# Performance work log

Hardware: AMD Instinct MI355X
Metric: run time of the kernel (lower is better)

Reference implementation:

```python
import jax, jax.numpy as jnp
import numpy as np

NUM_AGENTS = 8
OBSERVATION_SIZE = 30
INPUT_SHAPE = 4 + 2 * OBSERVATION_SIZE  # 64
STATE_SHAPE = INPUT_SHAPE * NUM_AGENTS  # 512
HYPER_HIDDEN_DIM = 40
QMIX_HIDDEN_DIM = 40


def setup_inputs() -> dict:
    key = jax.random.key(0)
    ks = jax.random.split(key, 16)
    E, T = 256, 256

    def lin(k, fan_in, fan_out):
        kw, kb = jax.random.split(k)
        bound = 1.0 / np.sqrt(fan_in)
        w = jax.random.uniform(kw, (fan_in, fan_out), jnp.float32, -bound, bound)
        b = jax.random.uniform(kb, (fan_out,), jnp.float32, -bound, bound)
        return w, b

    hw1_w0, hw1_b0 = lin(ks[0], STATE_SHAPE, HYPER_HIDDEN_DIM)
    hw1_w1, hw1_b1 = lin(ks[1], HYPER_HIDDEN_DIM, NUM_AGENTS * QMIX_HIDDEN_DIM)
    hw2_w0, hw2_b0 = lin(ks[2], STATE_SHAPE, HYPER_HIDDEN_DIM)
    hw2_w1, hw2_b1 = lin(ks[3], HYPER_HIDDEN_DIM, QMIX_HIDDEN_DIM)
    hb1_w, hb1_b = lin(ks[4], STATE_SHAPE, QMIX_HIDDEN_DIM)
    hb2_w0, hb2_b0 = lin(ks[5], STATE_SHAPE, QMIX_HIDDEN_DIM)
    hb2_w1, hb2_b1 = lin(ks[6], QMIX_HIDDEN_DIM, 1)

    return {
        "q_values": jax.random.normal(ks[7], (E, T, NUM_AGENTS), jnp.float32),
        "states": jax.random.normal(ks[8], (E, T, STATE_SHAPE), jnp.float32),
        "hw1_w0": hw1_w0, "hw1_b0": hw1_b0, "hw1_w1": hw1_w1, "hw1_b1": hw1_b1,
        "hw2_w0": hw2_w0, "hw2_b0": hw2_b0, "hw2_w1": hw2_w1, "hw2_b1": hw2_b1,
        "hb1_w": hb1_w, "hb1_b": hb1_b,
        "hb2_w0": hb2_w0, "hb2_b0": hb2_b0, "hb2_w1": hb2_w1, "hb2_b1": hb2_b1,
    }


def reference(q_values, states, hw1_w0, hw1_b0, hw1_w1, hw1_b1,
              hw2_w0, hw2_b0, hw2_w1, hw2_b1,
              hb1_w, hb1_b, hb2_w0, hb2_b0, hb2_w1, hb2_b1):
    E = q_values.shape[0]
    q = q_values.reshape(-1, NUM_AGENTS)          # [B, A]
    s = states.reshape(-1, STATE_SHAPE)           # [B, S]

    # hyper_w1: Linear-ReLU-Linear -> abs -> [B, A, H]
    w1 = jnp.abs(jax.nn.relu(s @ hw1_w0 + hw1_b0) @ hw1_w1 + hw1_b1)
    w1 = w1.reshape(-1, NUM_AGENTS, QMIX_HIDDEN_DIM)
    b1 = s @ hb1_w + hb1_b                        # [B, H]

    hidden = jax.nn.elu(jnp.einsum('ba,bah->bh', q, w1) + b1)  # [B, H]

    # hyper_w2 -> abs -> [B, H]; hyper_b2 -> [B, 1]
    w2 = jnp.abs(jax.nn.relu(s @ hw2_w0 + hw2_b0) @ hw2_w1 + hw2_b1)
    b2 = jax.nn.relu(s @ hb2_w0 + hb2_b0) @ hb2_w1 + hb2_b1    # [B, 1]

    q_total = jnp.einsum('bh,bh->b', hidden, w2)[:, None] + b2  # [B, 1]
    return q_total.reshape(E, -1, 1)
```

## Files before the change

### kernel.cpp

```cpp
#include <hip/hip_runtime.h>
#include <math.h>

#define NA 8
#define SS 512
#define N1 160
#define BROWS 32
#define NTHREADS 320

typedef __attribute__((ext_vector_type(8))) short bf16x8;
typedef __attribute__((ext_vector_type(4))) float f32x4;

static __device__ __forceinline__ unsigned short f2bf(float f) {
    union { float f; unsigned u; } v; v.f = f;
    unsigned r = v.u + 0x7FFFu + ((v.u >> 16) & 1u);
    return (unsigned short)(r >> 16);
}
static __device__ __forceinline__ float bf2f(unsigned short u) {
    union { unsigned u; float f; } v; v.u = ((unsigned)u) << 16; return v.f;
}

#define BP_OFF   0
#define BP1_OFF  81920
#define BP2_OFF  102400
#define BIAS0_BYTE 210944

__global__ void prep_kernel(const float* __restrict__ hw1_w0, const float* __restrict__ hb1_w,
                            const float* __restrict__ hw2_w0, const float* __restrict__ hb2_w0,
                            const float* __restrict__ hw1_w1, const float* __restrict__ hw2_w1,
                            const float* __restrict__ hw1_b0, const float* __restrict__ hb1_b,
                            const float* __restrict__ hw2_b0, const float* __restrict__ hb2_b0,
                            unsigned short* __restrict__ ws16, float* __restrict__ bias0) {
    int idx = blockIdx.x * blockDim.x + threadIdx.x;
    if (idx < 81920) {
        int i = idx & 7, l = (idx >> 3) & 63, t = idx >> 9;
        int kt = t & 15, nt = t >> 4;
        int k = kt * 32 + (l >> 4) * 8 + i;
        int n = nt * 16 + (l & 15);
        int seg = n / 40, c = n - seg * 40;
        const float* src = (seg == 0) ? hw1_w0 : (seg == 1) ? hb1_w : (seg == 2) ? hw2_w0 : hb2_w0;
        ws16[BP_OFF + idx] = f2bf(src[k * 40 + c]);
    } else if (idx < 81920 + 20480) {
        int j = idx - 81920;
        int i = j & 7, l = (j >> 3) & 63, t = j >> 9;
        int kt = t & 1, nt = t >> 1;
        int k = kt * 32 + (l >> 4) * 8 + i;
        int n = nt * 16 + (l & 15);
        float v = (k < 40) ? hw1_w1[k * 320 + n] : 0.f;
        ws16[BP1_OFF + j] = f2bf(v);
    } else if (idx < 81920 + 20480 + 3072) {
        int j = idx - 102400;
        int i = j & 7, l = (j >> 3) & 63, t = j >> 9;
        int kt = t & 1, nt = t >> 1;
        int k = kt * 32 + (l >> 4) * 8 + i;
        int n = nt * 16 + (l & 15);
        float v = (k < 40 && n < 40) ? hw2_w1[k * 40 + n] : 0.f;
        ws16[BP2_OFF + j] = f2bf(v);
    } else if (idx < 81920 + 20480 + 3072 + 160) {
        int j = idx - 105472;
        int seg = j / 40, c = j - seg * 40;
        const float* b = (seg == 0) ? hw1_b0 : (seg == 1) ? hb1_b : (seg == 2) ? hw2_b0 : hb2_b0;
        bias0[j] = b[c];
    }
}

#define REG0      0
#define P_OFF     32768
#define H1_OFF    53760
#define H2_OFF    57856
#define W2_OFF    61952
#define B2_OFF    64512
#define SMEM_BYTES 64640

__global__ __launch_bounds__(NTHREADS) void qmix_kernel(
    const float* __restrict__ q_values, const float* __restrict__ states,
    const unsigned short* __restrict__ Bp, const unsigned short* __restrict__ Bp1,
    const unsigned short* __restrict__ Bp2, const float* __restrict__ bias0,
    const float* __restrict__ hw1_b1, const float* __restrict__ hw2_b1,
    const float* __restrict__ hb2_w1, const float* __restrict__ hb2_b1,
    float* __restrict__ out)
{
    __shared__ __align__(16) char smem[SMEM_BYTES];
    const int tid = threadIdx.x;
    const int wv = tid >> 6;
    const int l = tid & 63;
    const int row0 = blockIdx.x * BROWS;

    {
        const float4* sg = (const float4*)(states + (size_t)row0 * SS);
        for (int idx = tid; idx < BROWS * (SS / 4); idx += NTHREADS) {
            int r = idx >> 7;
            int c4 = idx & 127;
            float4 v = sg[idx];
            ushort4 b;
            b.x = f2bf(v.x); b.y = f2bf(v.y); b.z = f2bf(v.z); b.w = f2bf(v.w);
            int byte = (r * 1024 + c4 * 8) ^ ((r & 7) << 4);
            *(ushort4*)(smem + byte) = b;
        }
    }
    __syncthreads();

    f32x4 acc[2][2] = {};
    {
        const int kch = (l >> 4) * 16;
        const int r0 = (l & 15);
        const int r1 = r0 + 16;
        const int swz0 = (r0 & 7) << 4;
        const unsigned short* bp0 = Bp + (size_t)((wv * 2 + 0) * 16) * 512 + (size_t)l * 8;
        const unsigned short* bp1 = Bp + (size_t)((wv * 2 + 1) * 16) * 512 + (size_t)l * 8;
        #pragma unroll
        for (int kt = 0; kt < 16; ++kt) {
            bf16x8 a0 = *(const bf16x8*)(smem + ((r0 * 1024 + kt * 64 + kch) ^ swz0));
            bf16x8 a1 = *(const bf16x8*)(smem + ((r1 * 1024 + kt * 64 + kch) ^ swz0));
            bf16x8 b0 = *(const bf16x8*)(bp0 + kt * 512);
            bf16x8 b1 = *(const bf16x8*)(bp1 + kt * 512);
            acc[0][0] = __builtin_amdgcn_mfma_f32_16x16x32_bf16(a0, b0, acc[0][0], 0, 0, 0);
            acc[0][1] = __builtin_amdgcn_mfma_f32_16x16x32_bf16(a0, b1, acc[0][1], 0, 0, 0);
            acc[1][0] = __builtin_amdgcn_mfma_f32_16x16x32_bf16(a1, b0, acc[1][0], 0, 0, 0);
            acc[1][1] = __builtin_amdgcn_mfma_f32_16x16x32_bf16(a1, b1, acc[1][1], 0, 0, 0);
        }
    }
    {
        float* P = (float*)(smem + P_OFF);
        #pragma unroll
        for (int mt = 0; mt < 2; ++mt)
        #pragma unroll
        for (int ntl = 0; ntl < 2; ++ntl)
        #pragma unroll
        for (int g = 0; g < 4; ++g) {
            int row = mt * 16 + (l >> 4) * 4 + g;
            int col = wv * 32 + ntl * 16 + (l & 15);
            P[row * 164 + col] = acc[mt][ntl][g];
        }
    }
    __syncthreads();

    {
        float* P = (float*)(smem + P_OFF);
        for (int idx = tid; idx < BROWS * N1; idx += NTHREADS) {
            int r = idx / N1, c = idx - r * N1;
            float v = P[r * 164 + c] + bias0[c];
            if ((unsigned)(c - 40) >= 40u) v = fmaxf(v, 0.f);
            P[r * 164 + c] = v;
        }
    }
    __syncthreads();

    {
        float* P = (float*)(smem + P_OFF);
        char* H1 = smem + H1_OFF;
        char* H2 = smem + H2_OFF;
        for (int idx = tid; idx < BROWS * 64; idx += NTHREADS) {
            int r = idx >> 6, j = idx & 63;
            float v1 = (j < 40) ? P[r * 164 + j] : 0.f;
            float v2 = (j < 40) ? P[r * 164 + 80 + j] : 0.f;
            int byte = (r * 128 + j * 2) ^ ((r & 7) << 4);
            *(unsigned short*)(H1 + byte) = f2bf(v1);
            *(unsigned short*)(H2 + byte) = f2bf(v2);
        }
        if (tid < 32) {
            float s = hb2_b1[0];
            #pragma unroll 8
            for (int j = 0; j < 40; ++j) s += P[tid * 164 + 120 + j] * hb2_w1[j];
            ((float*)(smem + B2_OFF))[tid] = s;
        }
    }
    __syncthreads();

    {
        char* H1 = smem + H1_OFF;
        const int kch = (l >> 4) * 16;
        f32x4 wacc[2][4] = {};
        #pragma unroll
        for (int kt = 0; kt < 2; ++kt) {
            bf16x8 a[2];
            #pragma unroll
            for (int mt = 0; mt < 2; ++mt) {
                int row = mt * 16 + (l & 15);
                a[mt] = *(const bf16x8*)(H1 + ((row * 128 + kt * 64 + kch) ^ ((row & 7) << 4)));
            }
            #pragma unroll
            for (int t = 0; t < 4; ++t) {
                int nt1 = wv * 4 + t;
                bf16x8 b = *(const bf16x8*)(Bp1 + ((size_t)(nt1 * 2 + kt) * 64 + l) * 8);
                wacc[0][t] = __builtin_amdgcn_mfma_f32_16x16x32_bf16(a[0], b, wacc[0][t], 0, 0, 0);
                wacc[1][t] = __builtin_amdgcn_mfma_f32_16x16x32_bf16(a[1], b, wacc[1][t], 0, 0, 0);
            }
        }
        unsigned short* W1 = (unsigned short*)(smem + REG0);
        #pragma unroll
        for (int mt = 0; mt < 2; ++mt)
        #pragma unroll
        for (int t = 0; t < 4; ++t)
        #pragma unroll
        for (int g = 0; g < 4; ++g) {
            int row = mt * 16 + (l >> 4) * 4 + g;
            int n = (wv * 4 + t) * 16 + (l & 15);
            W1[row * 320 + n] = f2bf(fabsf(wacc[mt][t][g] + hw1_b1[n]));
        }
        if (wv < 3) {
            char* H2 = smem + H2_OFF;
            f32x4 c2[2] = {};
            #pragma unroll
            for (int kt = 0; kt < 2; ++kt) {
                bf16x8 a[2];
                #pragma unroll
                for (int mt = 0; mt < 2; ++mt) {
                    int row = mt * 16 + (l & 15);
                    a[mt] = *(const bf16x8*)(H2 + ((row * 128 + kt * 64 + kch) ^ ((row & 7) << 4)));
                }
                bf16x8 b = *(const bf16x8*)(Bp2 + ((size_t)(wv * 2 + kt) * 64 + l) * 8);
                c2[0] = __builtin_amdgcn_mfma_f32_16x16x32_bf16(a[0], b, c2[0], 0, 0, 0);
                c2[1] = __builtin_amdgcn_mfma_f32_16x16x32_bf16(a[1], b, c2[1], 0, 0, 0);
            }
            unsigned short* W2 = (unsigned short*)(smem + W2_OFF);
            #pragma unroll
            for (int mt = 0; mt < 2; ++mt)
            #pragma unroll
            for (int g = 0; g < 4; ++g) {
                int row = mt * 16 + (l >> 4) * 4 + g;
                int n = wv * 16 + (l & 15);
                if (n < 40) W2[row * 40 + n] = f2bf(fabsf(c2[mt][g] + hw2_b1[n]));
            }
        }
    }
    __syncthreads();

    {
        float* P = (float*)(smem + P_OFF);
        unsigned short* W1 = (unsigned short*)(smem + REG0);
        unsigned short* W2 = (unsigned short*)(smem + W2_OFF);
        float* PR = (float*)(smem + H2_OFF);
        int r = tid / 10;
        int hb_ = tid - r * 10;
        const float4* qp = (const float4*)(q_values + (size_t)(row0 + r) * NA);
        float4 qa = qp[0], qb = qp[1];
        float qv[8] = {qa.x, qa.y, qa.z, qa.w, qb.x, qb.y, qb.z, qb.w};
        float psum = 0.f;
        #pragma unroll
        for (int kk = 0; kk < 4; ++kk) {
            int h = hb_ + kk * 10;
            float acc2 = P[r * 164 + 40 + h];
            #pragma unroll
            for (int a = 0; a < 8; ++a) acc2 += qv[a] * bf2f(W1[r * 320 + a * 40 + h]);
            float hid = (acc2 > 0.f) ? acc2 : expm1f(acc2);
            psum += hid * bf2f(W2[r * 40 + h]);
        }
        PR[tid] = psum;
    }
    __syncthreads();
    if (tid < 32) {
        float* PR = (float*)(smem + H2_OFF);
        float s = ((float*)(smem + B2_OFF))[tid];
        #pragma unroll
        for (int g = 0; g < 10; ++g) s += PR[tid * 10 + g];
        out[row0 + tid] = s;
    }
}

extern "C" void kernel_launch(void* const* d_in, const int* in_sizes, int n_in,
                              void* d_out, int out_size, void* d_ws, size_t ws_size,
                              hipStream_t stream) {
    const float* q_values = (const float*)d_in[0];
    const float* states   = (const float*)d_in[1];
    const float* hw1_w0 = (const float*)d_in[2];
    const float* hw1_b0 = (const float*)d_in[3];
    const float* hw1_w1 = (const float*)d_in[4];
    const float* hw1_b1 = (const float*)d_in[5];
    const float* hw2_w0 = (const float*)d_in[6];
    const float* hw2_b0 = (const float*)d_in[7];
    const float* hw2_w1 = (const float*)d_in[8];
    const float* hw2_b1 = (const float*)d_in[9];
    const float* hb1_w  = (const float*)d_in[10];
    const float* hb1_b  = (const float*)d_in[11];
    const float* hb2_w0 = (const float*)d_in[12];
    const float* hb2_b0 = (const float*)d_in[13];
    const float* hb2_w1 = (const float*)d_in[14];
    const float* hb2_b1 = (const float*)d_in[15];

    unsigned short* ws16 = (unsigned short*)d_ws;
    float* bias0 = (float*)((char*)d_ws + BIAS0_BYTE);

    const int prep_total = 81920 + 20480 + 3072 + 160;
    prep_kernel<<<(prep_total + 255) / 256, 256, 0, stream>>>(
        hw1_w0, hb1_w, hw2_w0, hb2_w0, hw1_w1, hw2_w1,
        hw1_b0, hb1_b, hw2_b0, hb2_b0, ws16, bias0);

    const int B = in_sizes[0] / NA;
    qmix_kernel<<<B / BROWS, NTHREADS, 0, stream>>>(
        q_values, states,
        ws16 + BP_OFF, ws16 + BP1_OFF, ws16 + BP2_OFF, bias0,
        hw1_b1, hw2_b1, hb2_w1, hb2_b1, (float*)d_out);
}
```

Measured before the change: 306.4 us.

## Fuse first-layer bias/ReLU epilogue into MFMA registers, drop P staging buffer

The first GEMM's accumulators now get bias, ReLU, bf16 conversion and the hb2 dot-product reduction applied directly from registers. The reduction uses wave shuffles and writes straight into the H1/H2/b1/B2 buffers. This removes the fp32 P staging matrix and two block-wide barriers with their passes over shared memory. It also shrinks shared memory and requests 4 blocks per CU via launch bounds to raise occupancy. The cost is branchy per-column epilogue code and a possible register cap from the launch-bounds hint.

```diff
diff --git a/kernel.cpp b/kernel.cpp
--- a/kernel.cpp
+++ b/kernel.cpp
@@ -3,7 +3,6 @@
 
 #define NA 8
 #define SS 512
-#define N1 160
 #define BROWS 32
 #define NTHREADS 320
 
@@ -63,15 +62,15 @@
     }
 }
 
-#define REG0      0
-#define P_OFF     32768
-#define H1_OFF    53760
-#define H2_OFF    57856
-#define W2_OFF    61952
-#define B2_OFF    64512
-#define SMEM_BYTES 64640
-
-__global__ __launch_bounds__(NTHREADS) void qmix_kernel(
+#define W1_STRIDE 324
+#define B1_OFF    32768
+#define H1_OFF    38400
+#define H2_OFF    42496
+#define W2_OFF    46592
+#define B2_OFF    49152
+#define SMEM_BYTES 49408
+
+__global__ __launch_bounds__(NTHREADS, 4) void qmix_kernel(
     const float* __restrict__ q_values, const float* __restrict__ states,
     const unsigned short* __restrict__ Bp, const unsigned short* __restrict__ Bp1,
     const unsigned short* __restrict__ Bp2, const float* __restrict__ bias0,
@@ -83,6 +82,7 @@
     const int tid = threadIdx.x;
     const int wv = tid >> 6;
     const int l = tid & 63;
+    const int p = l & 15;
     const int row0 = blockIdx.x * BROWS;
 
     {
@@ -96,13 +96,19 @@
             int byte = (r * 1024 + c4 * 8) ^ ((r & 7) << 4);
             *(ushort4*)(smem + byte) = b;
         }
+        for (int idx = tid; idx < 32 * 24; idx += NTHREADS) {
+            int r = idx / 24, k = 40 + (idx - r * 24);
+            int byte = (r * 128 + k * 2) ^ ((r & 7) << 4);
+            *(unsigned short*)(smem + H1_OFF + byte) = 0;
+            *(unsigned short*)(smem + H2_OFF + byte) = 0;
+        }
     }
     __syncthreads();
 
     f32x4 acc[2][2] = {};
     {
         const int kch = (l >> 4) * 16;
-        const int r0 = (l & 15);
+        const int r0 = p;
         const int r1 = r0 + 16;
         const int swz0 = (r0 & 7) << 4;
         const unsigned short* bp0 = Bp + (size_t)((wv * 2 + 0) * 16) * 512 + (size_t)l * 8;
@@ -119,49 +125,47 @@
             acc[1][1] = __builtin_amdgcn_mfma_f32_16x16x32_bf16(a1, b1, acc[1][1], 0, 0, 0);
         }
     }
-    {
-        float* P = (float*)(smem + P_OFF);
-        #pragma unroll
-        for (int mt = 0; mt < 2; ++mt)
-        #pragma unroll
-        for (int ntl = 0; ntl < 2; ++ntl)
-        #pragma unroll
-        for (int g = 0; g < 4; ++g) {
-            int row = mt * 16 + (l >> 4) * 4 + g;
-            int col = wv * 32 + ntl * 16 + (l & 15);
-            P[row * 164 + col] = acc[mt][ntl][g];
-        }
-    }
-    __syncthreads();
-
-    {
-        float* P = (float*)(smem + P_OFF);
-        for (int idx = tid; idx < BROWS * N1; idx += NTHREADS) {
-            int r = idx / N1, c = idx - r * N1;
-            float v = P[r * 164 + c] + bias0[c];
-            if ((unsigned)(c - 40) >= 40u) v = fmaxf(v, 0.f);
-            P[r * 164 + c] = v;
-        }
-    }
-    __syncthreads();
-
-    {
-        float* P = (float*)(smem + P_OFF);
-        char* H1 = smem + H1_OFF;
-        char* H2 = smem + H2_OFF;
-        for (int idx = tid; idx < BROWS * 64; idx += NTHREADS) {
-            int r = idx >> 6, j = idx & 63;
-            float v1 = (j < 40) ? P[r * 164 + j] : 0.f;
-            float v2 = (j < 40) ? P[r * 164 + 80 + j] : 0.f;
-            int byte = (r * 128 + j * 2) ^ ((r & 7) << 4);
-            *(unsigned short*)(H1 + byte) = f2bf(v1);
-            *(unsigned short*)(H2 + byte) = f2bf(v2);
-        }
-        if (tid < 32) {
-            float s = hb2_b1[0];
-            #pragma unroll 8
-            for (int j = 0; j < 40; ++j) s += P[tid * 164 + 120 + j] * hb2_w1[j];
-            ((float*)(smem + B2_OFF))[tid] = s;
+
+    {
+        float rs[2][4] = {{0.f,0.f,0.f,0.f},{0.f,0.f,0.f,0.f}};
+        float* b1buf = (float*)(smem + B1_OFF);
+        #pragma unroll
+        for (int ntl = 0; ntl < 2; ++ntl) {
+            const int c = wv * 32 + ntl * 16 + p;
+            const float bia = bias0[c];
+            const float hbw = (c >= 120) ? hb2_w1[c - 120] : 0.f;
+            #pragma unroll
+            for (int mt = 0; mt < 2; ++mt)
+            #pragma unroll
+            for (int g = 0; g < 4; ++g) {
+                const int row = mt * 16 + (l >> 4) * 4 + g;
+                const float v = acc[mt][ntl][g] + bia;
+                if (c < 40) {
+                    *(unsigned short*)(smem + H1_OFF + ((row * 128 + c * 2) ^ ((row & 7) << 4)))
+                        = f2bf(fmaxf(v, 0.f));
+                } else if (c < 80) {
+                    b1buf[row * 44 + (c - 40)] = v;
+                } else if (c < 120) {
+                    *(unsigned short*)(smem + H2_OFF + ((row * 128 + (c - 80) * 2) ^ ((row & 7) << 4)))
+                        = f2bf(fmaxf(v, 0.f));
+                } else {
+                    rs[mt][g] += fmaxf(v, 0.f) * hbw;
+                }
+            }
+        }
+        if (wv >= 3) {
+            float* B2 = (float*)(smem + B2_OFF);
+            #pragma unroll
+            for (int mt = 0; mt < 2; ++mt)
+            #pragma unroll
+            for (int g = 0; g < 4; ++g) {
+                float r2 = rs[mt][g];
+                r2 += __shfl_xor(r2, 1);
+                r2 += __shfl_xor(r2, 2);
+                r2 += __shfl_xor(r2, 4);
+                r2 += __shfl_xor(r2, 8);
+                if (p == 0) B2[(wv - 3) * 32 + mt * 16 + (l >> 4) * 4 + g] = r2;
+            }
         }
     }
     __syncthreads();
@@ -175,7 +179,7 @@
             bf16x8 a[2];
             #pragma unroll
             for (int mt = 0; mt < 2; ++mt) {
-                int row = mt * 16 + (l & 15);
+                int row = mt * 16 + p;
                 a[mt] = *(const bf16x8*)(H1 + ((row * 128 + kt * 64 + kch) ^ ((row & 7) << 4)));
             }
             #pragma unroll
@@ -186,7 +190,7 @@
                 wacc[1][t] = __builtin_amdgcn_mfma_f32_16x16x32_bf16(a[1], b, wacc[1][t], 0, 0, 0);
             }
         }
-        unsigned short* W1 = (unsigned short*)(smem + REG0);
+        unsigned short* W1 = (unsigned short*)smem;
         #pragma unroll
         for (int mt = 0; mt < 2; ++mt)
         #pragma unroll
@@ -194,8 +198,8 @@
         #pragma unroll
         for (int g = 0; g < 4; ++g) {
             int row = mt * 16 + (l >> 4) * 4 + g;
-            int n = (wv * 4 + t) * 16 + (l & 15);
-            W1[row * 320 + n] = f2bf(fabsf(wacc[mt][t][g] + hw1_b1[n]));
+            int n = (wv * 4 + t) * 16 + p;
+            W1[row * W1_STRIDE + n] = f2bf(fabsf(wacc[mt][t][g] + hw1_b1[n]));
         }
         if (wv < 3) {
             char* H2 = smem + H2_OFF;
@@ -205,7 +209,7 @@
                 bf16x8 a[2];
                 #pragma unroll
                 for (int mt = 0; mt < 2; ++mt) {
-                    int row = mt * 16 + (l & 15);
+                    int row = mt * 16 + p;
                     a[mt] = *(const bf16x8*)(H2 + ((row * 128 + kt * 64 + kch) ^ ((row & 7) << 4)));
                 }
                 bf16x8 b = *(const bf16x8*)(Bp2 + ((size_t)(wv * 2 + kt) * 64 + l) * 8);
@@ -218,7 +222,7 @@
             #pragma unroll
             for (int g = 0; g < 4; ++g) {
                 int row = mt * 16 + (l >> 4) * 4 + g;
-                int n = wv * 16 + (l & 15);
+                int n = wv * 16 + p;
                 if (n < 40) W2[row * 40 + n] = f2bf(fabsf(c2[mt][g] + hw2_b1[n]));
             }
         }
@@ -226,10 +230,10 @@
     __syncthreads();
 
     {
-        float* P = (float*)(smem + P_OFF);
-        unsigned short* W1 = (unsigned short*)(smem + REG0);
+        float* b1buf = (float*)(smem + B1_OFF);
+        unsigned short* W1 = (unsigned short*)smem;
         unsigned short* W2 = (unsigned short*)(smem + W2_OFF);
-        float* PR = (float*)(smem + H2_OFF);
+        float* PR = (float*)(smem + H1_OFF);
         int r = tid / 10;
         int hb_ = tid - r * 10;
         const float4* qp = (const float4*)(q_values + (size_t)(row0 + r) * NA);
@@ -239,9 +243,9 @@
         #pragma unroll
         for (int kk = 0; kk < 4; ++kk) {
             int h = hb_ + kk * 10;
-            float acc2 = P[r * 164 + 40 + h];
-            #pragma unroll
-            for (int a = 0; a < 8; ++a) acc2 += qv[a] * bf2f(W1[r * 320 + a * 40 + h]);
+            float acc2 = b1buf[r * 44 + h];
+            #pragma unroll
+            for (int a = 0; a < 8; ++a) acc2 += qv[a] * bf2f(W1[r * W1_STRIDE + a * 40 + h]);
             float hid = (acc2 > 0.f) ? acc2 : expm1f(acc2);
             psum += hid * bf2f(W2[r * 40 + h]);
         }
@@ -249,8 +253,9 @@
     }
     __syncthreads();
     if (tid < 32) {
-        float* PR = (float*)(smem + H2_OFF);
-        float s = ((float*)(smem + B2_OFF))[tid];
+        float* PR = (float*)(smem + H1_OFF);
+        float* B2 = (float*)(smem + B2_OFF);
+        float s = B2[tid] + B2[32 + tid] + hb2_b1[0];
         #pragma unroll
         for (int g = 0; g < 10; ++g) s += PR[tid * 10 + g];
         out[row0 + tid] = s;
```

After: 268.7 us. 1.14x faster.
